# Performance work log

Measured on AMD Instinct MI355X. Metric: run time of the kernel, lower is better.

## Reference

```python
import jax, jax.numpy as jnp
import numpy as np

NUM_HEADS = 8


def setup_inputs() -> dict:
    key = jax.random.key(0)
    k1, k2, k3 = jax.random.split(key, 3)
    B, C, H, W = 2, 256, 64, 64
    x = jax.random.normal(k1, (B, C, H, W), dtype=jnp.float32)
    # 1x1 conv kernels flattened to [out_ch, in_ch]
    w_qkv = jax.random.normal(k2, (3 * C, C), dtype=jnp.float32) * (1.0 / np.sqrt(C))
    w_proj = jax.random.normal(k3, (C, C), dtype=jnp.float32) * (1.0 / np.sqrt(C))
    return {"x": x, "w_qkv": w_qkv, "w_proj": w_proj}


def reference(x, w_qkv, w_proj):
    B, C, H, W = x.shape
    h = NUM_HEADS
    hc = C // h  # head_channels
    scale = hc ** (-0.5)

    # 1x1 conv == per-pixel matmul over channels
    qkv = jnp.einsum('bchw,oc->bohw', x, w_qkv)  # [B, 3C, H, W]
    q, k, v = jnp.split(qkv, 3, axis=1)          # each [B, C, H, W]

    def to_heads(t):
        # 'b (h c) x y -> b h (x y) c'
        return t.reshape(B, h, hc, H * W).transpose(0, 1, 3, 2)

    q, k, v = to_heads(q), to_heads(k), to_heads(v)  # [B, h, N, hc]

    attn = jax.nn.softmax(jnp.einsum('bhnc,bhmc->bhnm', q, k) * scale, axis=-1)
    out = jnp.einsum('bhnm,bhmc->bhnc', attn, v)     # [B, h, N, hc]

    # 'b h (x y) c -> b (h c) x y'
    out = out.transpose(0, 1, 3, 2).reshape(B, C, H, W)
    return jnp.einsum('bchw,oc->bohw', out, w_proj)
```

## Files before the change

### kernel.cpp

```cpp
#include <hip/hip_runtime.h>
#include <hip/hip_bf16.h>


typedef short s8v __attribute__((ext_vector_type(8)));
typedef float f32x16 __attribute__((ext_vector_type(16)));
typedef float f32x2 __attribute__((ext_vector_type(2)));
typedef unsigned int u32;
typedef unsigned int u32x4 __attribute__((ext_vector_type(4)));

__device__ __forceinline__ u32 cvt_pk_bf16(float lo, float hi){
  u32 d;
  asm("v_cvt_pk_bf16_f32 %0, %1, %2" : "=v"(d) : "v"(lo), "v"(hi));
  return d;
}

__device__ __forceinline__ int frag_off(int row, int c){
  return ((c>>4)<<9) + (((c>>3)&1)<<8) + (row<<3) + (c&7);
}

__global__ __launch_bounds__(256) void k_prep(const float* __restrict__ x,
                                              const float* __restrict__ wqkv,
                                              const float* __restrict__ wproj,
                                              __hip_bfloat16* __restrict__ xt,
                                              __hip_bfloat16* __restrict__ wq,
                                              __hip_bfloat16* __restrict__ wp){
  __shared__ float tile[64][65];
  const int b = blockIdx.z;
  const int c0 = blockIdx.y * 64, p0 = blockIdx.x * 64;
  const int tx = threadIdx.x & 63, ty = threadIdx.x >> 6;
  const float* src = x + ((size_t)b*256 + c0)*4096 + p0;
#pragma unroll
  for(int i=0;i<16;i++){
    int r = i*4 + ty;
    tile[r][tx] = src[(size_t)r*4096 + tx];
  }
  if(threadIdx.x < 64){
    int flat = (blockIdx.z*4 + blockIdx.y)*64 + blockIdx.x;
    int e = flat*64 + threadIdx.x;
    const float* srcw; __hip_bfloat16* dstw;
    if(e < 24576){ srcw = wqkv; dstw = wq; }
    else { e -= 24576; srcw = wproj; dstw = wp; }
    int o = e >> 5, cw = (e & 31)*8;
    const float* s = srcw + (size_t)o*256 + cw;
    u32x4 wv;
    wv.x = cvt_pk_bf16(s[0], s[1]);
    wv.y = cvt_pk_bf16(s[2], s[3]);
    wv.z = cvt_pk_bf16(s[4], s[5]);
    wv.w = cvt_pk_bf16(s[6], s[7]);
    *(u32x4*)(dstw + (size_t)(o>>5)*8192 + frag_off(o & 31, cw)) = wv;
  }
  __syncthreads();
  __hip_bfloat16* dstb = xt + (size_t)b*1048576;
#pragma unroll
  for(int it=0; it<2; ++it){
    int id = it*256 + threadIdx.x;
    int pl = id & 63, cc = id >> 6;
    int c = c0 + cc*8;
    u32x4 wv;
    wv.x = cvt_pk_bf16(tile[cc*8+0][pl], tile[cc*8+1][pl]);
    wv.y = cvt_pk_bf16(tile[cc*8+2][pl], tile[cc*8+3][pl]);
    wv.z = cvt_pk_bf16(tile[cc*8+4][pl], tile[cc*8+5][pl]);
    wv.w = cvt_pk_bf16(tile[cc*8+6][pl], tile[cc*8+7][pl]);
    int panel = (p0 + pl) >> 5;
    *(u32x4*)(dstb + (size_t)panel*8192 + frag_off(pl & 31, c)) = wv;
  }
}

__global__ __launch_bounds__(256) void k_qkv(const __hip_bfloat16* __restrict__ w,
                                             const __hip_bfloat16* __restrict__ xt,
                                             __hip_bfloat16* __restrict__ qb,
                                             __hip_bfloat16* __restrict__ kb,
                                             __hip_bfloat16* __restrict__ vt){
  const int wave = threadIdx.x >> 6, lane = threadIdx.x & 63;
  const int l31 = lane & 31, hi = lane >> 5;
  const int t = blockIdx.x*4 + wave;
  const int ntp = t & 127, mtp = t >> 7;
  const __hip_bfloat16* a0 = w  + (size_t)(2*mtp)*8192 + lane*8;
  const __hip_bfloat16* b0 = xt + (size_t)(2*ntp)*8192 + lane*8;
  f32x16 acc00, acc01, acc10, acc11;
#pragma unroll
  for(int i=0;i<16;i++){ acc00[i]=0.f; acc01[i]=0.f; acc10[i]=0.f; acc11[i]=0.f; }
  s8v af0 = *(const s8v*)a0,            af1 = *(const s8v*)(a0 + 8192);
  s8v bf0 = *(const s8v*)b0,            bf1 = *(const s8v*)(b0 + 8192);
  for(int kk=0;kk<15;kk++){
    const __hip_bfloat16* an = a0 + (kk+1)*512;
    const __hip_bfloat16* bn = b0 + (kk+1)*512;
    s8v na0 = *(const s8v*)an, na1 = *(const s8v*)(an + 8192);
    s8v nb0 = *(const s8v*)bn, nb1 = *(const s8v*)(bn + 8192);
    acc00 = __builtin_amdgcn_mfma_f32_32x32x16_bf16(af0, bf0, acc00, 0,0,0);
    acc01 = __builtin_amdgcn_mfma_f32_32x32x16_bf16(af0, bf1, acc01, 0,0,0);
    acc10 = __builtin_amdgcn_mfma_f32_32x32x16_bf16(af1, bf0, acc10, 0,0,0);
    acc11 = __builtin_amdgcn_mfma_f32_32x32x16_bf16(af1, bf1, acc11, 0,0,0);
    af0 = na0; af1 = na1; bf0 = nb0; bf1 = nb1;
  }
  acc00 = __builtin_amdgcn_mfma_f32_32x32x16_bf16(af0, bf0, acc00, 0,0,0);
  acc01 = __builtin_amdgcn_mfma_f32_32x32x16_bf16(af0, bf1, acc01, 0,0,0);
  acc10 = __builtin_amdgcn_mfma_f32_32x32x16_bf16(af1, bf0, acc10, 0,0,0);
  acc11 = __builtin_amdgcn_mfma_f32_32x32x16_bf16(af1, bf1, acc11, 0,0,0);

  const int region = mtp >> 2;
  const float s = (region==0) ? (0.17677669529663687f * 1.4426950408889634f) : 1.0f;
#pragma unroll
  for(int mi=0; mi<2; ++mi){
#pragma unroll
    for(int ni=0; ni<2; ++ni){
      const f32x16& acc = (mi==0) ? (ni==0?acc00:acc01) : (ni==0?acc10:acc11);
      const int mt = 2*mtp + mi, nt = 2*ntp + ni;
      const int bb = nt >> 7, ktile = nt & 127, h = mt & 7;
      const size_t tbase = (size_t)(bb*8 + h)*131072 + (size_t)ktile*1024;
      if(region < 2){
        __hip_bfloat16* dst = (region==0 ? qb : kb) + tbase + l31*8 + 4*hi;
#pragma unroll
        for(int g=0; g<4; ++g){
          uint2 wv;
          wv.x = cvt_pk_bf16(acc[4*g+0]*s, acc[4*g+1]*s);
          wv.y = cvt_pk_bf16(acc[4*g+2]*s, acc[4*g+3]*s);
          *(uint2*)(dst + (g>>1)*512 + (g&1)*256) = wv;
        }
      } else {
        const int j = l31 >> 4, hv = (l31 >> 2) & 1, tt = ((l31>>3)&1)*4 + (l31&3);
        __hip_bfloat16* dst = vt + tbase + j*512 + hv*256 + tt;
#pragma unroll
        for(int r=0;r<16;++r){
          int c = (r&3) + 8*(r>>2) + 4*hi;
          dst[c*8] = __float2bfloat16(acc[r]);
        }
      }
    }
  }
}

__global__ __launch_bounds__(256, 4) void k_attn(const __hip_bfloat16* __restrict__ qb,
                                                 const __hip_bfloat16* __restrict__ kb,
                                                 const __hip_bfloat16* __restrict__ vt,
                                                 __hip_bfloat16* __restrict__ ost){
  __shared__ float part[4][64][33];
  __shared__ float lsl[4][64];
  const int wave = threadIdx.x >> 6, lane = threadIdx.x & 63;
  const int l31 = lane & 31, hi = lane >> 5;
  const int vid = (blockIdx.x & 7)*128 + (blockIdx.x >> 3);
  const int bh = vid >> 6, qc = vid & 63;

  const __hip_bfloat16* qt = qb + (size_t)bh*131072 + (size_t)(qc*2)*1024 + (size_t)lane*8;
  const s8v qfA0 = *(const s8v*)qt;
  const s8v qfA1 = *(const s8v*)(qt + 512);
  const s8v qfB0 = *(const s8v*)(qt + 1024);
  const s8v qfB1 = *(const s8v*)(qt + 1536);

  const __hip_bfloat16* kp = kb + (size_t)bh*131072 + (size_t)(wave*32)*1024 + (size_t)lane*8;
  const __hip_bfloat16* vp = vt + (size_t)bh*131072 + (size_t)(wave*32)*1024 + (size_t)lane*8;

  f32x16 zf;
#pragma unroll
  for(int i=0;i<16;i++) zf[i]=0.f;
  f32x16 oaccA, oaccB;
#pragma unroll
  for(int i=0;i<16;i++){ oaccA[i]=0.f; oaccB[i]=0.f; }
  f32x2 sA0={0.f,0.f}, sA1={0.f,0.f}, sB0={0.f,0.f}, sB1={0.f,0.f};

  auto compute = [&](s8v kf0, s8v kf1, s8v vf0, s8v vf1){
    __builtin_amdgcn_s_setprio(1);
    f32x16 saA = __builtin_amdgcn_mfma_f32_32x32x16_bf16(kf0, qfA0, zf, 0,0,0);
    saA = __builtin_amdgcn_mfma_f32_32x32x16_bf16(kf1, qfA1, saA, 0,0,0);
    f32x16 saB = __builtin_amdgcn_mfma_f32_32x32x16_bf16(kf0, qfB0, zf, 0,0,0);
    saB = __builtin_amdgcn_mfma_f32_32x32x16_bf16(kf1, qfB1, saB, 0,0,0);
    __builtin_amdgcn_s_setprio(0);
    float pvA[16], pvB[16];
#pragma unroll
    for(int r=0;r<16;++r) pvA[r] = __builtin_amdgcn_exp2f(saA[r]);
#pragma unroll
    for(int r=0;r<16;++r) pvB[r] = __builtin_amdgcn_exp2f(saB[r]);
    sA0 += (f32x2){pvA[0],pvA[1]};   sA1 += (f32x2){pvA[2],pvA[3]};
    sA0 += (f32x2){pvA[4],pvA[5]};   sA1 += (f32x2){pvA[6],pvA[7]};
    sA0 += (f32x2){pvA[8],pvA[9]};   sA1 += (f32x2){pvA[10],pvA[11]};
    sA0 += (f32x2){pvA[12],pvA[13]}; sA1 += (f32x2){pvA[14],pvA[15]};
    sB0 += (f32x2){pvB[0],pvB[1]};   sB1 += (f32x2){pvB[2],pvB[3]};
    sB0 += (f32x2){pvB[4],pvB[5]};   sB1 += (f32x2){pvB[6],pvB[7]};
    sB0 += (f32x2){pvB[8],pvB[9]};   sB1 += (f32x2){pvB[10],pvB[11]};
    sB0 += (f32x2){pvB[12],pvB[13]}; sB1 += (f32x2){pvB[14],pvB[15]};

    u32x4 wA0, wA1, wB0, wB1;
    wA0.x = cvt_pk_bf16(pvA[0],  pvA[1]);   wA0.y = cvt_pk_bf16(pvA[2],  pvA[3]);
    wA0.z = cvt_pk_bf16(pvA[4],  pvA[5]);   wA0.w = cvt_pk_bf16(pvA[6],  pvA[7]);
    wA1.x = cvt_pk_bf16(pvA[8],  pvA[9]);   wA1.y = cvt_pk_bf16(pvA[10], pvA[11]);
    wA1.z = cvt_pk_bf16(pvA[12], pvA[13]);  wA1.w = cvt_pk_bf16(pvA[14], pvA[15]);
    wB0.x = cvt_pk_bf16(pvB[0],  pvB[1]);   wB0.y = cvt_pk_bf16(pvB[2],  pvB[3]);
    wB0.z = cvt_pk_bf16(pvB[4],  pvB[5]);   wB0.w = cvt_pk_bf16(pvB[6],  pvB[7]);
    wB1.x = cvt_pk_bf16(pvB[8],  pvB[9]);   wB1.y = cvt_pk_bf16(pvB[10], pvB[11]);
    wB1.z = cvt_pk_bf16(pvB[12], pvB[13]);  wB1.w = cvt_pk_bf16(pvB[14], pvB[15]);

    __builtin_amdgcn_s_setprio(1);
    oaccA = __builtin_amdgcn_mfma_f32_32x32x16_bf16(vf0, __builtin_bit_cast(s8v, wA0), oaccA, 0,0,0);
    oaccA = __builtin_amdgcn_mfma_f32_32x32x16_bf16(vf1, __builtin_bit_cast(s8v, wA1), oaccA, 0,0,0);
    oaccB = __builtin_amdgcn_mfma_f32_32x32x16_bf16(vf0, __builtin_bit_cast(s8v, wB0), oaccB, 0,0,0);
    oaccB = __builtin_amdgcn_mfma_f32_32x32x16_bf16(vf1, __builtin_bit_cast(s8v, wB1), oaccB, 0,0,0);
    __builtin_amdgcn_s_setprio(0);
  };

  s8v kf0 = *(const s8v*)kp, kf1 = *(const s8v*)(kp + 512);
  s8v vf0 = *(const s8v*)vp, vf1 = *(const s8v*)(vp + 512);
  for(int i=0;i<31;++i){
    const __hip_bfloat16* nkp = kp + (i+1)*1024;
    const __hip_bfloat16* nvp = vp + (i+1)*1024;
    s8v nk0 = *(const s8v*)nkp, nk1 = *(const s8v*)(nkp + 512);
    s8v nv0 = *(const s8v*)nvp, nv1 = *(const s8v*)(nvp + 512);
    compute(kf0, kf1, vf0, vf1);
    kf0 = nk0; kf1 = nk1; vf0 = nv0; vf1 = nv1;
  }
  compute(kf0, kf1, vf0, vf1);

  float lsumA = (sA0.x + sA0.y) + (sA1.x + sA1.y);
  float lsumB = (sB0.x + sB0.y) + (sB1.x + sB1.y);
  lsumA += __shfl_xor(lsumA, 32, 64);
  lsumB += __shfl_xor(lsumB, 32, 64);
  lsl[wave][l31] = lsumA;
  lsl[wave][32 + l31] = lsumB;
#pragma unroll
  for(int r=0;r<16;++r){
    int c = (r&3) + 8*(r>>2) + 4*hi;
    part[wave][l31][c] = oaccA[r];
    part[wave][32 + l31][c] = oaccB[r];
  }
  __syncthreads();

  const int b = bh >> 3, h = bh & 7;
  __hip_bfloat16* obase = ost + (size_t)(b*128 + qc*2)*8192;
#pragma unroll
  for(int it=0; it<8; ++it){
    int e = it*256 + threadIdx.x;
    int q = e >> 5, c = e & 31;
    float o = (part[0][q][c] + part[1][q][c]) + (part[2][q][c] + part[3][q][c]);
    float L = (lsl[0][q] + lsl[1][q]) + (lsl[2][q] + lsl[3][q]);
    obase[(size_t)(q>>5)*8192 + (h*2 + (c>>4))*512 + ((c>>3)&1)*256 + (q&31)*8 + (c&7)]
        = __float2bfloat16(o / L);
  }
}

__global__ __launch_bounds__(256) void k_proj(const __hip_bfloat16* __restrict__ w,
                                              const __hip_bfloat16* __restrict__ ost,
                                              float* __restrict__ out){
  const int wave = threadIdx.x >> 6, lane = threadIdx.x & 63;
  const int l31 = lane & 31, hi = lane >> 5;
  const int t = blockIdx.x*4 + wave;
  const int nt = t & 255, mt = t >> 8;
  const __hip_bfloat16* arow = w   + (size_t)mt*8192 + lane*8;
  const __hip_bfloat16* brow = ost + (size_t)nt*8192 + lane*8;
  f32x16 acc;
#pragma unroll
  for(int i=0;i<16;i++) acc[i]=0.f;
  s8v a = *(const s8v*)arow, b = *(const s8v*)brow;
  for(int kk=0;kk<15;kk++){
    s8v na = *(const s8v*)(arow + (kk+1)*512);
    s8v nb = *(const s8v*)(brow + (kk+1)*512);
    acc = __builtin_amdgcn_mfma_f32_32x32x16_bf16(a, b, acc, 0,0,0);
    a = na; b = nb;
  }
  acc = __builtin_amdgcn_mfma_f32_32x32x16_bf16(a, b, acc, 0,0,0);
  const int pg = nt*32 + l31;
  const int bb = pg >> 12, p = pg & 4095;
  float* dst = out + (size_t)bb*1048576 + p;
#pragma unroll
  for(int r=0;r<16;++r){
    int o = mt*32 + (r&3) + 8*(r>>2) + 4*hi;
    dst[(size_t)o*4096] = acc[r];
  }
}

extern "C" void kernel_launch(void* const* d_in, const int* in_sizes, int n_in,
                              void* d_out, int out_size, void* d_ws, size_t ws_size,
                              hipStream_t stream){
  const float* x     = (const float*)d_in[0];
  const float* wqkv  = (const float*)d_in[1];
  const float* wproj = (const float*)d_in[2];
  float* out = (float*)d_out;

  const size_t SZ_XT = (size_t)8192*256*2;
  const size_t SZ_VT = (size_t)16*32*4096*2;
  const size_t SZ_WQ = (size_t)768*256*2;
  const size_t SZ_WP = (size_t)256*256*2;
  if(ws_size < SZ_XT + SZ_VT + SZ_WQ + SZ_WP) return;

  char* ws = (char*)d_ws;
  __hip_bfloat16* xt  = (__hip_bfloat16*)ws;
  __hip_bfloat16* vt  = (__hip_bfloat16*)(ws + SZ_XT);
  __hip_bfloat16* wqb = (__hip_bfloat16*)(ws + SZ_XT + SZ_VT);
  __hip_bfloat16* wpb = (__hip_bfloat16*)(ws + SZ_XT + SZ_VT + SZ_WQ);
  __hip_bfloat16* qb  = (__hip_bfloat16*)d_out;
  __hip_bfloat16* kb  = qb + (size_t)2*1024*1024;
  __hip_bfloat16* ost = xt;

  k_prep<<<dim3(64,4,2), 256, 0, stream>>>(x, wqkv, wproj, xt, wqb, wpb);
  k_qkv<<<384, 256, 0, stream>>>(wqb, xt, qb, kb, vt);
  k_attn<<<1024, 256, 0, stream>>>(qb, kb, vt, ost);
  k_proj<<<512, 256, 0, stream>>>(wpb, ost, out);
}
```

Measured before the change: 71.99 us.

## Process four query tiles per attention block to reuse K/V loads

Each attention block now handles 128 queries (four 32-row tiles) instead of 64, so each K/V fragment loaded from memory feeds four QK and PV MFMA chains. The grid is halved to 512 blocks and the cross-wave reduction runs in two passes through the shared buffer. The explicit software prefetch of the next K/V tile is dropped, the s_setprio hints are removed, and the launch-bounds occupancy hint is relaxed. Together these raise register pressure and may lower occupancy and load-latency hiding.

Result: slower. 84.56 us (+17.5%).

```diff
diff --git a/kernel.cpp b/kernel.cpp
--- a/kernel.cpp
+++ b/kernel.cpp
@@ -130,22 +130,24 @@
   }
 }
 
-__global__ __launch_bounds__(256, 4) void k_attn(const __hip_bfloat16* __restrict__ qb,
-                                                 const __hip_bfloat16* __restrict__ kb,
-                                                 const __hip_bfloat16* __restrict__ vt,
-                                                 __hip_bfloat16* __restrict__ ost){
+__global__ __launch_bounds__(256) void k_attn(const __hip_bfloat16* __restrict__ qb,
+                                              const __hip_bfloat16* __restrict__ kb,
+                                              const __hip_bfloat16* __restrict__ vt,
+                                              __hip_bfloat16* __restrict__ ost){
   __shared__ float part[4][64][33];
-  __shared__ float lsl[4][64];
+  __shared__ float lsl[4][128];
   const int wave = threadIdx.x >> 6, lane = threadIdx.x & 63;
   const int l31 = lane & 31, hi = lane >> 5;
-  const int vid = (blockIdx.x & 7)*128 + (blockIdx.x >> 3);
-  const int bh = vid >> 6, qc = vid & 63;
-
-  const __hip_bfloat16* qt = qb + (size_t)bh*131072 + (size_t)(qc*2)*1024 + (size_t)lane*8;
-  const s8v qfA0 = *(const s8v*)qt;
-  const s8v qfA1 = *(const s8v*)(qt + 512);
-  const s8v qfB0 = *(const s8v*)(qt + 1024);
-  const s8v qfB1 = *(const s8v*)(qt + 1536);
+  const int vid = (blockIdx.x & 7)*64 + (blockIdx.x >> 3);
+  const int bh = vid >> 5, qc = vid & 31;
+
+  const __hip_bfloat16* qt = qb + (size_t)bh*131072 + (size_t)(qc*4)*1024 + (size_t)lane*8;
+  s8v qf0[4], qf1[4];
+#pragma unroll
+  for(int t=0;t<4;++t){
+    qf0[t] = *(const s8v*)(qt + t*1024);
+    qf1[t] = *(const s8v*)(qt + t*1024 + 512);
+  }
 
   const __hip_bfloat16* kp = kb + (size_t)bh*131072 + (size_t)(wave*32)*1024 + (size_t)lane*8;
   const __hip_bfloat16* vp = vt + (size_t)bh*131072 + (size_t)(wave*32)*1024 + (size_t)lane*8;
@@ -153,86 +155,74 @@
   f32x16 zf;
 #pragma unroll
   for(int i=0;i<16;i++) zf[i]=0.f;
-  f32x16 oaccA, oaccB;
-#pragma unroll
-  for(int i=0;i<16;i++){ oaccA[i]=0.f; oaccB[i]=0.f; }
-  f32x2 sA0={0.f,0.f}, sA1={0.f,0.f}, sB0={0.f,0.f}, sB1={0.f,0.f};
-
-  auto compute = [&](s8v kf0, s8v kf1, s8v vf0, s8v vf1){
-    __builtin_amdgcn_s_setprio(1);
-    f32x16 saA = __builtin_amdgcn_mfma_f32_32x32x16_bf16(kf0, qfA0, zf, 0,0,0);
-    saA = __builtin_amdgcn_mfma_f32_32x32x16_bf16(kf1, qfA1, saA, 0,0,0);
-    f32x16 saB = __builtin_amdgcn_mfma_f32_32x32x16_bf16(kf0, qfB0, zf, 0,0,0);
-    saB = __builtin_amdgcn_mfma_f32_32x32x16_bf16(kf1, qfB1, saB, 0,0,0);
-    __builtin_amdgcn_s_setprio(0);
-    float pvA[16], pvB[16];
-#pragma unroll
-    for(int r=0;r<16;++r) pvA[r] = __builtin_amdgcn_exp2f(saA[r]);
-#pragma unroll
-    for(int r=0;r<16;++r) pvB[r] = __builtin_amdgcn_exp2f(saB[r]);
-    sA0 += (f32x2){pvA[0],pvA[1]};   sA1 += (f32x2){pvA[2],pvA[3]};
-    sA0 += (f32x2){pvA[4],pvA[5]};   sA1 += (f32x2){pvA[6],pvA[7]};
-    sA0 += (f32x2){pvA[8],pvA[9]};   sA1 += (f32x2){pvA[10],pvA[11]};
-    sA0 += (f32x2){pvA[12],pvA[13]}; sA1 += (f32x2){pvA[14],pvA[15]};
-    sB0 += (f32x2){pvB[0],pvB[1]};   sB1 += (f32x2){pvB[2],pvB[3]};
-    sB0 += (f32x2){pvB[4],pvB[5]};   sB1 += (f32x2){pvB[6],pvB[7]};
-    sB0 += (f32x2){pvB[8],pvB[9]};   sB1 += (f32x2){pvB[10],pvB[11]};
-    sB0 += (f32x2){pvB[12],pvB[13]}; sB1 += (f32x2){pvB[14],pvB[15]};
-
-    u32x4 wA0, wA1, wB0, wB1;
-    wA0.x = cvt_pk_bf16(pvA[0],  pvA[1]);   wA0.y = cvt_pk_bf16(pvA[2],  pvA[3]);
-    wA0.z = cvt_pk_bf16(pvA[4],  pvA[5]);   wA0.w = cvt_pk_bf16(pvA[6],  pvA[7]);
-    wA1.x = cvt_pk_bf16(pvA[8],  pvA[9]);   wA1.y = cvt_pk_bf16(pvA[10], pvA[11]);
-    wA1.z = cvt_pk_bf16(pvA[12], pvA[13]);  wA1.w = cvt_pk_bf16(pvA[14], pvA[15]);
-    wB0.x = cvt_pk_bf16(pvB[0],  pvB[1]);   wB0.y = cvt_pk_bf16(pvB[2],  pvB[3]);
-    wB0.z = cvt_pk_bf16(pvB[4],  pvB[5]);   wB0.w = cvt_pk_bf16(pvB[6],  pvB[7]);
-    wB1.x = cvt_pk_bf16(pvB[8],  pvB[9]);   wB1.y = cvt_pk_bf16(pvB[10], pvB[11]);
-    wB1.z = cvt_pk_bf16(pvB[12], pvB[13]);  wB1.w = cvt_pk_bf16(pvB[14], pvB[15]);
-
-    __builtin_amdgcn_s_setprio(1);
-    oaccA = __builtin_amdgcn_mfma_f32_32x32x16_bf16(vf0, __builtin_bit_cast(s8v, wA0), oaccA, 0,0,0);
-    oaccA = __builtin_amdgcn_mfma_f32_32x32x16_bf16(vf1, __builtin_bit_cast(s8v, wA1), oaccA, 0,0,0);
-    oaccB = __builtin_amdgcn_mfma_f32_32x32x16_bf16(vf0, __builtin_bit_cast(s8v, wB0), oaccB, 0,0,0);
-    oaccB = __builtin_amdgcn_mfma_f32_32x32x16_bf16(vf1, __builtin_bit_cast(s8v, wB1), oaccB, 0,0,0);
-    __builtin_amdgcn_s_setprio(0);
-  };
-
-  s8v kf0 = *(const s8v*)kp, kf1 = *(const s8v*)(kp + 512);
-  s8v vf0 = *(const s8v*)vp, vf1 = *(const s8v*)(vp + 512);
-  for(int i=0;i<31;++i){
-    const __hip_bfloat16* nkp = kp + (i+1)*1024;
-    const __hip_bfloat16* nvp = vp + (i+1)*1024;
-    s8v nk0 = *(const s8v*)nkp, nk1 = *(const s8v*)(nkp + 512);
-    s8v nv0 = *(const s8v*)nvp, nv1 = *(const s8v*)(nvp + 512);
-    compute(kf0, kf1, vf0, vf1);
-    kf0 = nk0; kf1 = nk1; vf0 = nv0; vf1 = nv1;
-  }
-  compute(kf0, kf1, vf0, vf1);
-
-  float lsumA = (sA0.x + sA0.y) + (sA1.x + sA1.y);
-  float lsumB = (sB0.x + sB0.y) + (sB1.x + sB1.y);
-  lsumA += __shfl_xor(lsumA, 32, 64);
-  lsumB += __shfl_xor(lsumB, 32, 64);
-  lsl[wave][l31] = lsumA;
-  lsl[wave][32 + l31] = lsumB;
-#pragma unroll
-  for(int r=0;r<16;++r){
-    int c = (r&3) + 8*(r>>2) + 4*hi;
-    part[wave][l31][c] = oaccA[r];
-    part[wave][32 + l31][c] = oaccB[r];
-  }
-  __syncthreads();
+  f32x16 oacc[4];
+#pragma unroll
+  for(int t=0;t<4;++t)
+#pragma unroll
+    for(int i=0;i<16;i++) oacc[t][i]=0.f;
+  f32x2 s0[4], s1[4];
+#pragma unroll
+  for(int t=0;t<4;++t){ s0[t]=(f32x2){0.f,0.f}; s1[t]=(f32x2){0.f,0.f}; }
+
+  for(int i=0;i<32;++i){
+    const __hip_bfloat16* kpi = kp + (size_t)i*1024;
+    const __hip_bfloat16* vpi = vp + (size_t)i*1024;
+    s8v kf0 = *(const s8v*)kpi, kf1 = *(const s8v*)(kpi + 512);
+    s8v vf0 = *(const s8v*)vpi, vf1 = *(const s8v*)(vpi + 512);
+#pragma unroll
+    for(int t=0;t<4;++t){
+      f32x16 sa = __builtin_amdgcn_mfma_f32_32x32x16_bf16(kf0, qf0[t], zf, 0,0,0);
+      sa = __builtin_amdgcn_mfma_f32_32x32x16_bf16(kf1, qf1[t], sa, 0,0,0);
+      float pv[16];
+#pragma unroll
+      for(int r=0;r<16;++r) pv[r] = __builtin_amdgcn_exp2f(sa[r]);
+      s0[t] += (f32x2){pv[0],pv[1]};   s1[t] += (f32x2){pv[2],pv[3]};
+      s0[t] += (f32x2){pv[4],pv[5]};   s1[t] += (f32x2){pv[6],pv[7]};
+      s0[t] += (f32x2){pv[8],pv[9]};   s1[t] += (f32x2){pv[10],pv[11]};
+      s0[t] += (f32x2){pv[12],pv[13]}; s1[t] += (f32x2){pv[14],pv[15]};
+      u32x4 w0, w1;
+      w0.x = cvt_pk_bf16(pv[0],  pv[1]);   w0.y = cvt_pk_bf16(pv[2],  pv[3]);
+      w0.z = cvt_pk_bf16(pv[4],  pv[5]);   w0.w = cvt_pk_bf16(pv[6],  pv[7]);
+      w1.x = cvt_pk_bf16(pv[8],  pv[9]);   w1.y = cvt_pk_bf16(pv[10], pv[11]);
+      w1.z = cvt_pk_bf16(pv[12], pv[13]);  w1.w = cvt_pk_bf16(pv[14], pv[15]);
+      oacc[t] = __builtin_amdgcn_mfma_f32_32x32x16_bf16(vf0, __builtin_bit_cast(s8v, w0), oacc[t], 0,0,0);
+      oacc[t] = __builtin_amdgcn_mfma_f32_32x32x16_bf16(vf1, __builtin_bit_cast(s8v, w1), oacc[t], 0,0,0);
+    }
+  }
+
+#pragma unroll
+  for(int t=0;t<4;++t){
+    float ls = (s0[t].x + s0[t].y) + (s1[t].x + s1[t].y);
+    ls += __shfl_xor(ls, 32, 64);
+    lsl[wave][t*32 + l31] = ls;
+  }
 
   const int b = bh >> 3, h = bh & 7;
-  __hip_bfloat16* obase = ost + (size_t)(b*128 + qc*2)*8192;
-#pragma unroll
-  for(int it=0; it<8; ++it){
-    int e = it*256 + threadIdx.x;
-    int q = e >> 5, c = e & 31;
-    float o = (part[0][q][c] + part[1][q][c]) + (part[2][q][c] + part[3][q][c]);
-    float L = (lsl[0][q] + lsl[1][q]) + (lsl[2][q] + lsl[3][q]);
-    obase[(size_t)(q>>5)*8192 + (h*2 + (c>>4))*512 + ((c>>3)&1)*256 + (q&31)*8 + (c&7)]
-        = __float2bfloat16(o / L);
+  __hip_bfloat16* obase = ost + (size_t)(b*128 + qc*4)*8192;
+
+#pragma unroll
+  for(int p=0;p<2;++p){
+    if(p) __syncthreads();
+#pragma unroll
+    for(int u=0;u<2;++u){
+      const f32x16& oa = oacc[2*p + u];
+#pragma unroll
+      for(int r=0;r<16;++r){
+        int c = (r&3) + 8*(r>>2) + 4*hi;
+        part[wave][u*32 + l31][c] = oa[r];
+      }
+    }
+    __syncthreads();
+#pragma unroll
+    for(int it=0; it<8; ++it){
+      int e = it*256 + threadIdx.x;
+      int q = e >> 5, c = e & 31;
+      float o = (part[0][q][c] + part[1][q][c]) + (part[2][q][c] + part[3][q][c]);
+      int qg = 2*p*32 + q;
+      float L = (lsl[0][qg] + lsl[1][qg]) + (lsl[2][qg] + lsl[3][qg]);
+      obase[(size_t)(qg>>5)*8192 + (h*2 + (c>>4))*512 + ((c>>3)&1)*256 + (qg&31)*8 + (c&7)]
+          = __float2bfloat16(o / L);
+    }
   }
 }
 
@@ -291,6 +281,6 @@
 
   k_prep<<<dim3(64,4,2), 256, 0, stream>>>(x, wqkv, wproj, xt, wqb, wpb);
   k_qkv<<<384, 256, 0, stream>>>(wqb, xt, qb, kb, vt);
-  k_attn<<<1024, 256, 0, stream>>>(qb, kb, vt, ost);
+  k_attn<<<512, 256, 0, stream>>>(qb, kb, vt, ost);
   k_proj<<<512, 256, 0, stream>>>(wpb, ost, out);
 }
```
